# Performance work log

Hardware: AMD Instinct MI355X
Metric: run time of the kernel (lower is better)

## Reference

```python
import jax, jax.numpy as jnp
import numpy as np

N_NODES = 100000
N_EDGE_PAIRS = 800000  # undirected pairs -> 1.6M directed edges
DIM_IN = 128
NUM_CLASSES = 16
N_ITERS = 5


def _log_normalize(a):
    return a - jax.nn.logsumexp(a, axis=-1, keepdims=True)


def setup_inputs() -> dict:
    key = jax.random.key(0)
    k1, k2, k3, k4, k5 = jax.random.split(key, 5)
    # reciprocal directed edges: edges 2i and 2i+1 are reverses of each other
    src = jax.random.randint(k1, (N_EDGE_PAIRS,), 0, N_NODES)
    dst = jax.random.randint(k2, (N_EDGE_PAIRS,), 0, N_NODES)
    e_src = jnp.stack([src, dst], axis=1).reshape(-1)  # [E]
    e_dst = jnp.stack([dst, src], axis=1).reshape(-1)  # [E]
    edge_index = jnp.stack([e_src, e_dst], axis=0)     # [2, E]
    E = e_src.shape[0]
    rv = jnp.arange(E).reshape(-1, 2)[:, ::-1].reshape(-1)  # reverse-edge permutation
    x = jax.random.normal(k3, (N_NODES, DIM_IN), dtype=jnp.float32)
    W = jax.random.normal(k4, (DIM_IN, NUM_CLASSES), dtype=jnp.float32) * 0.1
    b = jnp.zeros((NUM_CLASSES,), dtype=jnp.float32)
    dim_param = NUM_CLASSES * (NUM_CLASSES + 1) // 2
    param = jax.random.normal(k5, (dim_param,), dtype=jnp.float32) * 0.1
    return {"x": x, "W": W, "b": b, "param": param,
            "edge_index": edge_index, "rv": rv}


def reference(x, W, b, param, edge_index, rv):
    N = x.shape[0]
    C = W.shape[1]
    # MLP (num_hidden=0 -> single Linear) + LogSoftmax
    log_b0 = jax.nn.log_softmax(x @ W + b, axis=-1)  # [N, C]
    # coupling matrix logH (symmetric), detached since learn_coupling=False
    rid, cid = np.tril_indices(C)
    logT = jnp.zeros((C, C), dtype=x.dtype).at[rid, cid].set(
        jax.nn.log_sigmoid(param * 10.0))
    logH = logT + jnp.triu(logT.T, 1)
    logH = jax.lax.stop_gradient(logH)
    src, dst = edge_index[0], edge_index[1]
    E = src.shape[0]
    log_msg = jnp.full((E, C), -float(np.log(C)), dtype=x.dtype)
    log_b = log_b0
    for _ in range(N_ITERS):
        # message: gather beliefs at source, subtract reverse message
        t = log_b[src] - log_msg[rv]                                    # [E, C]
        raw = jax.nn.logsumexp(t[:, :, None] + logH[None, :, :], axis=1)  # [E, C]
        log_msg = _log_normalize(raw)
        # aggregate (scatter-add) into destination nodes, then update
        agg = jax.ops.segment_sum(log_msg, dst, num_segments=N)         # [N, C]
        log_b = _log_normalize(agg + log_b0)
    return log_b
```

## Files before the change

kernel.cpp:

```cpp
#include <hip/hip_runtime.h>
#include <hip/hip_fp16.h>
#include <math.h>

#define NN      100000
#define EE      1600000
#define NPAIRS  800000
#define DIN     128
#define CC      16
#define NITERS  5
#define UU      4
#define NBLKS   (NPAIRS / 8)
#define GRID_E  (NBLKS / (UU * 4))
#define NEGLOGC (-2.772588722239781f)
#define FPSCALE 1048576.0f
#define FPINV   (1.0f / 1048576.0f)

#if __has_builtin(__builtin_amdgcn_mfma_f32_16x16x16bf16_1k)
#define USE_1K 1
#else
#define USE_1K 0
#endif

typedef float f4  __attribute__((ext_vector_type(4)));
typedef float v4f __attribute__((ext_vector_type(4)));
typedef short v4s __attribute__((ext_vector_type(4)));
typedef short v8s __attribute__((ext_vector_type(8)));
typedef unsigned int u4v __attribute__((ext_vector_type(4)));
typedef int  i4v __attribute__((ext_vector_type(4)));
typedef unsigned long long ull;

__device__ __forceinline__ unsigned short f2h(float f) {
    return __half_as_ushort(__float2half(f));
}
__device__ __forceinline__ float h2f(unsigned short u) {
    return __half2float(__ushort_as_half(u));
}
__device__ __forceinline__ unsigned int pack_h(float lo, float hi) {
    return (unsigned int)f2h(lo) | ((unsigned int)f2h(hi) << 16);
}
__device__ __forceinline__ unsigned short f2bf(float f) {
    unsigned int u = __float_as_uint(f);
    unsigned int r = u + 0x7fffu + ((u >> 16) & 1u);
    return (unsigned short)(r >> 16);
}

__global__ __launch_bounds__(256) void k_setup(
    const float* __restrict__ x, const float* __restrict__ W,
    const float* __restrict__ b, const float* __restrict__ param,
    float* __restrict__ M, float* __restrict__ logb0,
    unsigned int* __restrict__ agg32)
{
    if (blockIdx.x == 0 && threadIdx.x < CC * (CC + 1) / 2) {
        int i = threadIdx.x;
        int r = 0;
        while ((r + 1) * (r + 2) / 2 <= i) ++r;
        int c = i - r * (r + 1) / 2;
        float z = param[i] * 10.0f;
        float s = 1.0f / (1.0f + __expf(-z));
        M[r * CC + c] = s;
        if (r != c) M[c * CC + r] = s;
    }

    int idx = blockIdx.x * 256 + threadIdx.x;
    agg32[idx] = 0u;

    int node = idx >> 4;
    int cls  = idx & 15;
    const f4* xr4 = (const f4*)(x + (long)node * DIN);
    float acc = b[cls];
#pragma unroll 8
    for (int k4 = 0; k4 < DIN / 4; ++k4) {
        f4 xv = __builtin_nontemporal_load(xr4 + k4);
        acc = fmaf(xv.x, W[(4 * k4 + 0) * CC + cls], acc);
        acc = fmaf(xv.y, W[(4 * k4 + 1) * CC + cls], acc);
        acc = fmaf(xv.z, W[(4 * k4 + 2) * CC + cls], acc);
        acc = fmaf(xv.w, W[(4 * k4 + 3) * CC + cls], acc);
    }
    float m = acc;
    for (int off = 8; off; off >>= 1) m = fmaxf(m, __shfl_xor(m, off, 16));
    float s = __expf(acc - m);
    for (int off = 8; off; off >>= 1) s += __shfl_xor(s, off, 16);
    logb0[idx] = acc - m - __logf(s);
}

template <bool RD_MSG, bool WR_MSG>
__global__ __launch_bounds__(256) void k_edges_m(
    const int* __restrict__ esrc, const int* __restrict__ edst,
    const float* __restrict__ logb, const float* __restrict__ Mg,
    unsigned int* __restrict__ msg2, ull* __restrict__ agg8)
{
    const int lane = threadIdx.x & 63;
    const int wid  = blockIdx.x * 4 + (threadIdx.x >> 6);
    const int m    = lane & 15;
    const int q    = lane >> 4;

#if USE_1K
    v4s bfrag;
#pragma unroll
    for (int j = 0; j < 4; ++j)
        bfrag[j] = (short)f2bf(Mg[(4 * q + j) * CC + m]);
#else
    v8s bfrag = {0, 0, 0, 0, 0, 0, 0, 0};
    if (q < 2) {
#pragma unroll
        for (int j = 0; j < 8; ++j)
            bfrag[j] = (short)f2bf(Mg[(8 * q + j) * CC + m]);
    }
#endif

#pragma unroll
    for (int u = 0; u < UU; ++u) {
        const int  blk = wid * UU + u;
        const long eb  = (long)blk * 16;
        const long pb  = (long)blk * 8;
        const long p   = pb + (m >> 1);

        int src = __builtin_nontemporal_load(esrc + eb + m);

        v4f acc = {0.f, 0.f, 0.f, 0.f};
        v4f D;
#if USE_1K
        f4 lb = *(const f4*)(logb + (long)src * CC + 4 * q);
        float mo[4];
        if (RD_MSG) {
            u4v mw = __builtin_nontemporal_load(
                (const u4v*)(msg2 + p * CC + 4 * q));
#pragma unroll
            for (int j = 0; j < 4; ++j)
                mo[j] = (m & 1) ? h2f((unsigned short)(mw[j] & 0xffffu))
                                : h2f((unsigned short)(mw[j] >> 16));
        } else {
#pragma unroll
            for (int j = 0; j < 4; ++j) mo[j] = NEGLOGC;
        }
        v4s a;
#pragma unroll
        for (int j = 0; j < 4; ++j)
            a[j] = (short)f2bf(__expf(lb[j] - mo[j]));
        D = __builtin_amdgcn_mfma_f32_16x16x16bf16_1k(a, bfrag, acc, 0, 0, 0);
#else
        v8s a = {0, 0, 0, 0, 0, 0, 0, 0};
        if (q < 2) {
            f4 lbA = *(const f4*)(logb + (long)src * CC + 8 * q);
            f4 lbB = *(const f4*)(logb + (long)src * CC + 8 * q + 4);
            float mo[8];
            if (RD_MSG) {
                u4v mwA = __builtin_nontemporal_load(
                    (const u4v*)(msg2 + p * CC + 8 * q));
                u4v mwB = __builtin_nontemporal_load(
                    (const u4v*)(msg2 + p * CC + 8 * q + 4));
#pragma unroll
                for (int j = 0; j < 4; ++j) {
                    mo[j]     = (m & 1) ? h2f((unsigned short)(mwA[j] & 0xffffu))
                                        : h2f((unsigned short)(mwA[j] >> 16));
                    mo[4 + j] = (m & 1) ? h2f((unsigned short)(mwB[j] & 0xffffu))
                                        : h2f((unsigned short)(mwB[j] >> 16));
                }
            } else {
#pragma unroll
                for (int j = 0; j < 8; ++j) mo[j] = NEGLOGC;
            }
#pragma unroll
            for (int j = 0; j < 4; ++j) {
                a[j]     = (short)f2bf(__expf(lbA[j] - mo[j]));
                a[4 + j] = (short)f2bf(__expf(lbB[j] - mo[4 + j]));
            }
        }
        D = __builtin_amdgcn_mfma_f32_16x16x32_bf16(a, bfrag, acc, 0, 0, 0);
#endif

        v4f T = D;
#pragma unroll
        for (int off = 1; off < 16; off <<= 1) {
#pragma unroll
            for (int i = 0; i < 4; ++i) T[i] += __shfl_xor(T[i], off, 16);
        }
        float n0 = __logf(D[0]) - __logf(T[0]);
        float n1 = __logf(D[1]) - __logf(T[1]);
        float n2 = __logf(D[2]) - __logf(T[2]);
        float n3 = __logf(D[3]) - __logf(T[3]);

        if (WR_MSG) {
            __builtin_nontemporal_store(pack_h(n0, n1),
                                        msg2 + (pb + 2 * q) * CC + m);
            __builtin_nontemporal_store(pack_h(n2, n3),
                                        msg2 + (pb + 2 * q + 1) * CC + m);
        }

        i4v d4 = *(const i4v*)(edst + eb + 4 * q);
        float nv[4] = {n0, n1, n2, n3};
#pragma unroll
        for (int i = 0; i < 4; ++i) {
            unsigned int qv = (unsigned int)(fmaxf(-nv[i], 0.f) * FPSCALE + 0.5f);
            unsigned int pv = __shfl_xor(qv, 1, 16);
            if (!(m & 1)) {
                ull val = (ull)qv | ((ull)pv << 32);
                atomicAdd(&agg8[(long)d4[i] * 8 + (m >> 1)], val);
            }
        }
    }
}

__global__ __launch_bounds__(256) void k_update(
    const float* __restrict__ logb0, unsigned int* __restrict__ agg32,
    float* __restrict__ out)
{
    int idx = blockIdx.x * blockDim.x + threadIdx.x;
    unsigned int q = agg32[idx];
    agg32[idx] = 0u;
    float v = fmaf(-(float)q, FPINV, logb0[idx]);
    float m = v;
    for (int off = 8; off; off >>= 1) m = fmaxf(m, __shfl_xor(m, off, 16));
    float s = __expf(v - m);
    for (int off = 8; off; off >>= 1) s += __shfl_xor(s, off, 16);
    out[idx] = v - m - __logf(s);
}

extern "C" void kernel_launch(void* const* d_in, const int* in_sizes, int n_in,
                              void* d_out, int out_size, void* d_ws, size_t ws_size,
                              hipStream_t stream)
{
    const float* x     = (const float*)d_in[0];
    const float* W     = (const float*)d_in[1];
    const float* b     = (const float*)d_in[2];
    const float* param = (const float*)d_in[3];
    const int*   eidx  = (const int*)d_in[4];
    const int*   esrc  = eidx;
    const int*   edst  = eidx + EE;

    float* ws    = (float*)d_ws;
    float* M     = ws;
    float* logb0 = M     + 256;
    float* logb  = logb0 + (long)NN * CC;
    unsigned int* agg32 = (unsigned int*)(logb + (long)NN * CC);
    ull*          agg8  = (ull*)agg32;
    unsigned int* msg2  = agg32 + (long)NN * CC;

    k_setup<<<NN * CC / 256, 256, 0, stream>>>(x, W, b, param, M, logb0, agg32);

    const float* curb = logb0;
    for (int it = 0; it < NITERS; ++it) {
        if (it == 0)
            k_edges_m<false, true><<<GRID_E, 256, 0, stream>>>(
                esrc, edst, curb, M, msg2, agg8);
        else if (it == NITERS - 1)
            k_edges_m<true, false><<<GRID_E, 256, 0, stream>>>(
                esrc, edst, curb, M, msg2, agg8);
        else
            k_edges_m<true, true><<<GRID_E, 256, 0, stream>>>(
                esrc, edst, curb, M, msg2, agg8);
        float* dst = (it == NITERS - 1) ? (float*)d_out : logb;
        k_update<<<NN * CC / 256, 256, 0, stream>>>(logb0, agg32, dst);
        curb = dst;
    }
}
```

Baseline: 574.1 us.

## Compute message normalizer from precomputed H row sums and batch edge loads up front

Precomputes the row sums of the coupling matrix in setup, so each edge's normalizing total is a dot product of the exp values with those sums. This replaces the 16-lane butterfly reduction after the MFMA with a cheap two-step cross-quadrant shuffle plus a broadcast. The per-edge index, message and belief loads for all UU blocks are also issued before any compute, so their latency can overlap. This raises register pressure, and the normalizer is now taken from fp32 values rather than the bf16 MFMA output, which changes rounding slightly.

New measurement: 573.3 us. No clear change (-0.1%).

```diff
diff --git a/kernel.cpp b/kernel.cpp
--- a/kernel.cpp
+++ b/kernel.cpp
@@ -50,15 +50,23 @@
     float* __restrict__ M, float* __restrict__ logb0,
     unsigned int* __restrict__ agg32)
 {
-    if (blockIdx.x == 0 && threadIdx.x < CC * (CC + 1) / 2) {
-        int i = threadIdx.x;
-        int r = 0;
-        while ((r + 1) * (r + 2) / 2 <= i) ++r;
-        int c = i - r * (r + 1) / 2;
-        float z = param[i] * 10.0f;
-        float s = 1.0f / (1.0f + __expf(-z));
-        M[r * CC + c] = s;
-        if (r != c) M[c * CC + r] = s;
+    if (blockIdx.x == 0) {
+        if (threadIdx.x < CC * (CC + 1) / 2) {
+            int i = threadIdx.x;
+            int r = 0;
+            while ((r + 1) * (r + 2) / 2 <= i) ++r;
+            int c = i - r * (r + 1) / 2;
+            float z = param[i] * 10.0f;
+            float s = 1.0f / (1.0f + __expf(-z));
+            M[r * CC + c] = s;
+            if (r != c) M[c * CC + r] = s;
+        }
+        __syncthreads();
+        if (threadIdx.x < CC) {
+            float s = 0.f;
+            for (int c = 0; c < CC; ++c) s += M[threadIdx.x * CC + c];
+            M[256 + threadIdx.x] = s;
+        }
     }
 
     int idx = blockIdx.x * 256 + threadIdx.x;
@@ -99,6 +107,74 @@
 #pragma unroll
     for (int j = 0; j < 4; ++j)
         bfrag[j] = (short)f2bf(Mg[(4 * q + j) * CC + m]);
+    f4 rs = *(const f4*)(Mg + 256 + 4 * q);
+
+    int src[UU];
+    i4v d4[UU];
+    u4v mw[UU];
+    f4  lb[UU];
+#pragma unroll
+    for (int u = 0; u < UU; ++u) {
+        const long eb = (long)(wid * UU + u) * 16;
+        src[u] = __builtin_nontemporal_load(esrc + eb + m);
+        d4[u]  = *(const i4v*)(edst + eb + 4 * q);
+    }
+#pragma unroll
+    for (int u = 0; u < UU; ++u) {
+        const long p = (long)(wid * UU + u) * 8 + (m >> 1);
+        if (RD_MSG)
+            mw[u] = __builtin_nontemporal_load((const u4v*)(msg2 + p * CC + 4 * q));
+        lb[u] = *(const f4*)(logb + (long)src[u] * CC + 4 * q);
+    }
+
+#pragma unroll
+    for (int u = 0; u < UU; ++u) {
+        const long pb = (long)(wid * UU + u) * 8;
+
+        float e[4], Tm = 0.f;
+#pragma unroll
+        for (int j = 0; j < 4; ++j) {
+            float mo = NEGLOGC;
+            if (RD_MSG)
+                mo = (m & 1) ? h2f((unsigned short)(mw[u][j] & 0xffffu))
+                             : h2f((unsigned short)(mw[u][j] >> 16));
+            e[j] = __expf(lb[u][j] - mo);
+            Tm   = fmaf(e[j], rs[j], Tm);
+        }
+        Tm += __shfl_xor(Tm, 16, 64);
+        Tm += __shfl_xor(Tm, 32, 64);
+        float ltA = __logf(Tm);
+
+        v4s a;
+#pragma unroll
+        for (int j = 0; j < 4; ++j) a[j] = (short)f2bf(e[j]);
+        v4f acc = {0.f, 0.f, 0.f, 0.f};
+        v4f D = __builtin_amdgcn_mfma_f32_16x16x16bf16_1k(a, bfrag, acc, 0, 0, 0);
+
+        float n[4];
+#pragma unroll
+        for (int i = 0; i < 4; ++i) {
+            float lT = __shfl(ltA, 4 * q + i, 16);
+            n[i] = __logf(D[i]) - lT;
+        }
+
+        if (WR_MSG) {
+            __builtin_nontemporal_store(pack_h(n[0], n[1]),
+                                        msg2 + (pb + 2 * q) * CC + m);
+            __builtin_nontemporal_store(pack_h(n[2], n[3]),
+                                        msg2 + (pb + 2 * q + 1) * CC + m);
+        }
+
+#pragma unroll
+        for (int i = 0; i < 4; ++i) {
+            unsigned int qv = (unsigned int)(fmaxf(-n[i], 0.f) * FPSCALE + 0.5f);
+            unsigned int pv = __shfl_xor(qv, 1, 16);
+            if (!(m & 1)) {
+                ull val = (ull)qv | ((ull)pv << 32);
+                atomicAdd(&agg8[(long)d4[u][i] * 8 + (m >> 1)], val);
+            }
+        }
+    }
 #else
     v8s bfrag = {0, 0, 0, 0, 0, 0, 0, 0};
     if (q < 2) {
@@ -106,49 +182,21 @@
         for (int j = 0; j < 8; ++j)
             bfrag[j] = (short)f2bf(Mg[(8 * q + j) * CC + m]);
     }
-#endif
-
 #pragma unroll
     for (int u = 0; u < UU; ++u) {
         const int  blk = wid * UU + u;
         const long eb  = (long)blk * 16;
         const long pb  = (long)blk * 8;
         const long p   = pb + (m >> 1);
-
         int src = __builtin_nontemporal_load(esrc + eb + m);
-
-        v4f acc = {0.f, 0.f, 0.f, 0.f};
-        v4f D;
-#if USE_1K
-        f4 lb = *(const f4*)(logb + (long)src * CC + 4 * q);
-        float mo[4];
-        if (RD_MSG) {
-            u4v mw = __builtin_nontemporal_load(
-                (const u4v*)(msg2 + p * CC + 4 * q));
-#pragma unroll
-            for (int j = 0; j < 4; ++j)
-                mo[j] = (m & 1) ? h2f((unsigned short)(mw[j] & 0xffffu))
-                                : h2f((unsigned short)(mw[j] >> 16));
-        } else {
-#pragma unroll
-            for (int j = 0; j < 4; ++j) mo[j] = NEGLOGC;
-        }
-        v4s a;
-#pragma unroll
-        for (int j = 0; j < 4; ++j)
-            a[j] = (short)f2bf(__expf(lb[j] - mo[j]));
-        D = __builtin_amdgcn_mfma_f32_16x16x16bf16_1k(a, bfrag, acc, 0, 0, 0);
-#else
         v8s a = {0, 0, 0, 0, 0, 0, 0, 0};
         if (q < 2) {
             f4 lbA = *(const f4*)(logb + (long)src * CC + 8 * q);
             f4 lbB = *(const f4*)(logb + (long)src * CC + 8 * q + 4);
             float mo[8];
             if (RD_MSG) {
-                u4v mwA = __builtin_nontemporal_load(
-                    (const u4v*)(msg2 + p * CC + 8 * q));
-                u4v mwB = __builtin_nontemporal_load(
-                    (const u4v*)(msg2 + p * CC + 8 * q + 4));
+                u4v mwA = __builtin_nontemporal_load((const u4v*)(msg2 + p * CC + 8 * q));
+                u4v mwB = __builtin_nontemporal_load((const u4v*)(msg2 + p * CC + 8 * q + 4));
 #pragma unroll
                 for (int j = 0; j < 4; ++j) {
                     mo[j]     = (m & 1) ? h2f((unsigned short)(mwA[j] & 0xffffu))
@@ -166,32 +214,25 @@
                 a[4 + j] = (short)f2bf(__expf(lbB[j] - mo[4 + j]));
             }
         }
-        D = __builtin_amdgcn_mfma_f32_16x16x32_bf16(a, bfrag, acc, 0, 0, 0);
-#endif
-
+        v4f acc = {0.f, 0.f, 0.f, 0.f};
+        v4f D = __builtin_amdgcn_mfma_f32_16x16x32_bf16(a, bfrag, acc, 0, 0, 0);
         v4f T = D;
 #pragma unroll
         for (int off = 1; off < 16; off <<= 1) {
 #pragma unroll
             for (int i = 0; i < 4; ++i) T[i] += __shfl_xor(T[i], off, 16);
         }
-        float n0 = __logf(D[0]) - __logf(T[0]);
-        float n1 = __logf(D[1]) - __logf(T[1]);
-        float n2 = __logf(D[2]) - __logf(T[2]);
-        float n3 = __logf(D[3]) - __logf(T[3]);
-
+        float n[4];
+#pragma unroll
+        for (int i = 0; i < 4; ++i) n[i] = __logf(D[i]) - __logf(T[i]);
         if (WR_MSG) {
-            __builtin_nontemporal_store(pack_h(n0, n1),
-                                        msg2 + (pb + 2 * q) * CC + m);
-            __builtin_nontemporal_store(pack_h(n2, n3),
-                                        msg2 + (pb + 2 * q + 1) * CC + m);
-        }
-
+            __builtin_nontemporal_store(pack_h(n[0], n[1]), msg2 + (pb + 2 * q) * CC + m);
+            __builtin_nontemporal_store(pack_h(n[2], n[3]), msg2 + (pb + 2 * q + 1) * CC + m);
+        }
         i4v d4 = *(const i4v*)(edst + eb + 4 * q);
-        float nv[4] = {n0, n1, n2, n3};
 #pragma unroll
         for (int i = 0; i < 4; ++i) {
-            unsigned int qv = (unsigned int)(fmaxf(-nv[i], 0.f) * FPSCALE + 0.5f);
+            unsigned int qv = (unsigned int)(fmaxf(-n[i], 0.f) * FPSCALE + 0.5f);
             unsigned int pv = __shfl_xor(qv, 1, 16);
             if (!(m & 1)) {
                 ull val = (ull)qv | ((ull)pv << 32);
@@ -199,6 +240,7 @@
             }
         }
     }
+#endif
 }
 
 __global__ __launch_bounds__(256) void k_update(
@@ -230,7 +272,7 @@
 
     float* ws    = (float*)d_ws;
     float* M     = ws;
-    float* logb0 = M     + 256;
+    float* logb0 = M     + 288;
     float* logb  = logb0 + (long)NN * CC;
     unsigned int* agg32 = (unsigned int*)(logb + (long)NN * CC);
     ull*          agg8  = (ull*)agg32;
```
